# Performance work log

Hardware: AMD Instinct MI355X
Metric: run time of the kernel (lower is better)

Reference implementation:

```python
import jax, jax.numpy as jnp
import numpy as np

INPUT_DIM = 2048
OUT_DIM = 4096
DEGREE = 3          # repo's 'degree' arg; acts as spline ORDER (recursion depth degree-1)
N_KNOTS = 64
N_COEF = N_KNOTS - DEGREE  # 61, matches c.shape[-1]


def bspline_basis(x, t, order):
    """Vectorized Cox-de Boor. x: (I,), t: (K,) -> basis (I, K - order).

    Degree-0 indicators then `order-1` recursion steps, matching the
    original per-scalar recursive cox_deboor(c, t, order, x) whose output
    length is n_knots - order (== c.shape[-1]).
    """
    xk = x[:, None]  # (I, 1)
    # B_{k,0}(x) = 1 if t[k] <= x < t[k+1]   -> (I, K-1)
    B = ((t[None, :-1] <= xk) & (xk < t[None, 1:])).astype(x.dtype)
    for p in range(1, order):
        # left:  (x - t[k]) / (t[k+p] - t[k])
        left = (xk - t[None, : -(p + 1)]) / (t[p:-1] - t[: -(p + 1)])[None, :]
        # right: (t[k+p+1] - x) / (t[k+p+1] - t[k+1])
        right = (t[None, p + 1 :] - xk) / (t[p + 1 :] - t[1 : t.shape[0] - p])[None, :]
        B = left * B[:, :-1] + right * B[:, 1:]
    return B  # (I, K - order)


def setup_inputs() -> dict:
    key = jax.random.key(0)
    kx, kc = jax.random.split(key)
    x = jax.random.uniform(kx, (INPUT_DIM,), dtype=jnp.float32)  # in [0,1) c [-1,1]
    c = jax.random.normal(kc, (INPUT_DIM, OUT_DIM, N_COEF), dtype=jnp.float32)
    return {"x": x, "c": c}


def reference(x, c):
    t = jnp.linspace(-1.0, 1.0, N_KNOTS, dtype=x.dtype)
    B = bspline_basis(x, t, DEGREE)           # (I, N_COEF)
    # out[j] = sum_i sum_k c[i,j,k] * B[i,k]
    return jnp.einsum("iok,ik->o", c, B)       # (OUT_DIM,)
```

## Files before the change

### kernel.cpp

```cpp
#include <hip/hip_runtime.h>
#include <math.h>


#define INPUT_DIM 2048
#define OUT_DIM   4096
#define N_COEF    61
#define IC        16
#define OB        256

__device__ __forceinline__ float Tk(int k) {
    return -1.0f + (float)k * (2.0f / 63.0f);
}

__global__ void kan_zero_kernel(float* __restrict__ out) {
    out[blockIdx.x * blockDim.x + threadIdx.x] = 0.0f;
}

__global__ __launch_bounds__(OB) void kan_kernel(const float* __restrict__ x,
                                                 const float* __restrict__ c,
                                                 float* __restrict__ out) {
    __shared__ int    sk0[IC];
    __shared__ float4 sw[IC];

    const int tid    = threadIdx.x;
    const int i_base = blockIdx.y * IC;

    if (tid < IC) {
        const float xv = x[i_base + tid];
        int j = (int)floorf((xv + 1.0f) * 31.5f);
        j = max(0, min(62, j));
        while (j > 0  && xv <  Tk(j))     --j;
        while (j < 62 && xv >= Tk(j + 1)) ++j;

        const float tjm1 = Tk(j - 1), tj = Tk(j), tj1 = Tk(j + 1), tj2 = Tk(j + 2);
        const float b1l = (tj1 - xv) / (tj1 - tj);
        const float b1r = (xv - tj)  / (tj1 - tj);
        const float w0 = (tj1 - xv) / (tj1 - tjm1) * b1l;
        const float w1 = (xv - tjm1) / (tj1 - tjm1) * b1l
                       + (tj2 - xv) / (tj2 - tj)    * b1r;
        const float w2 = (xv - tj)  / (tj2 - tj)    * b1r;

        int s = j - 59; if (s < 0) s = 0;
        int k0 = j - 2 - s; if (k0 < 0) k0 = 0;
        const float wsrc[3] = {w0, w1, w2};
        float ww[4] = {0.0f, 0.0f, 0.0f, 0.0f};
        #pragma unroll
        for (int m = 0; m < 3; ++m) {
            const int l = (j - 2 + m) - k0;
            if (0 <= l && l < 4) ww[l] = wsrc[m];
        }
        sk0[tid] = k0;
        sw[tid]  = make_float4(ww[0], ww[1], ww[2], ww[3]);
    }
    __syncthreads();

    const int o = blockIdx.x * OB + tid;
    const long long stride_i = (long long)OUT_DIM * N_COEF;
    const float* pbase = c + (long long)i_base * stride_i + (long long)o * N_COEF;

    float4 d[IC];
    #pragma unroll
    for (int ii = 0; ii < IC; ++ii) {
        const float* p = pbase + (long long)ii * stride_i + sk0[ii];
        d[ii] = *reinterpret_cast<const float4*>(p);
    }

    float acc = 0.0f;
    #pragma unroll
    for (int ii = 0; ii < IC; ++ii) {
        const float4 w = sw[ii];
        acc = fmaf(d[ii].x, w.x, acc);
        acc = fmaf(d[ii].y, w.y, acc);
        acc = fmaf(d[ii].z, w.z, acc);
        acc = fmaf(d[ii].w, w.w, acc);
    }
    atomicAdd(&out[o], acc);
}

extern "C" void kernel_launch(void* const* d_in, const int* in_sizes, int n_in,
                              void* d_out, int out_size, void* d_ws, size_t ws_size,
                              hipStream_t stream) {
    const float* x   = (const float*)d_in[0];
    const float* c   = (const float*)d_in[1];
    float*       out = (float*)d_out;

    hipLaunchKernelGGL(kan_zero_kernel, dim3(OUT_DIM / 256), dim3(256), 0, stream, out);

    dim3 grid(OUT_DIM / OB, INPUT_DIM / IC);
    hipLaunchKernelGGL(kan_kernel, grid, dim3(OB), 0, stream, x, c, out);
}
```

Baseline: 2.356 ms.

## Stream full coefficient chunks through LDS with coalesced loads instead of sparse gathers

Replaces the per-thread sparse float4 gather of 4 coefficients (strided by 61 floats) with a fully coalesced copy of each 256x61 coefficient chunk into shared memory, then reads the 4 needed values from LDS. It also doubles the input rows per block from 16 to 32, which halves the number of atomics. The gather wasted sector bandwidth and coalescing, but the new version reads all 61 coefficients per output instead of about 4, roughly 15x more DRAM traffic. It also adds two barriers per row with no overlap between loading and compute.

New measurement: 2.668 ms. 1.13x slower.

```diff
diff --git a/kernel.cpp b/kernel.cpp
--- a/kernel.cpp
+++ b/kernel.cpp
@@ -5,8 +5,10 @@
 #define INPUT_DIM 2048
 #define OUT_DIM   4096
 #define N_COEF    61
-#define IC        16
 #define OB        256
+#define IG        32
+#define CHUNK_F   (OB * N_COEF)
+#define CHUNK_V4  (CHUNK_F / 4)
 
 __device__ __forceinline__ float Tk(int k) {
     return -1.0f + (float)k * (2.0f / 63.0f);
@@ -19,13 +21,15 @@
 __global__ __launch_bounds__(OB) void kan_kernel(const float* __restrict__ x,
                                                  const float* __restrict__ c,
                                                  float* __restrict__ out) {
-    __shared__ int    sk0[IC];
-    __shared__ float4 sw[IC];
+    __shared__ float4 ldsv[CHUNK_V4];
+    __shared__ int    sk0[IG];
+    __shared__ float4 sw[IG];
 
     const int tid    = threadIdx.x;
-    const int i_base = blockIdx.y * IC;
+    const int o0     = blockIdx.x * OB;
+    const int i_base = blockIdx.y * IG;
 
-    if (tid < IC) {
+    if (tid < IG) {
         const float xv = x[i_base + tid];
         int j = (int)floorf((xv + 1.0f) * 31.5f);
         j = max(0, min(62, j));
@@ -54,27 +58,28 @@
     }
     __syncthreads();
 
-    const int o = blockIdx.x * OB + tid;
-    const long long stride_i = (long long)OUT_DIM * N_COEF;
-    const float* pbase = c + (long long)i_base * stride_i + (long long)o * N_COEF;
+    const float* ldsf = (const float*)ldsv;
+    float acc = 0.0f;
 
-    float4 d[IC];
-    #pragma unroll
-    for (int ii = 0; ii < IC; ++ii) {
-        const float* p = pbase + (long long)ii * stride_i + sk0[ii];
-        d[ii] = *reinterpret_cast<const float4*>(p);
+    for (int ii = 0; ii < IG; ++ii) {
+        const float4* src = (const float4*)(c + ((long long)(i_base + ii) * OUT_DIM + o0)
+                                                  * (long long)N_COEF);
+        for (int idx = tid; idx < CHUNK_V4; idx += OB) {
+            ldsv[idx] = src[idx];
+        }
+        __syncthreads();
+
+        const int    k0 = sk0[ii];
+        const float4 w  = sw[ii];
+        const float* row = ldsf + tid * N_COEF + k0;
+        acc = fmaf(row[0], w.x, acc);
+        acc = fmaf(row[1], w.y, acc);
+        acc = fmaf(row[2], w.z, acc);
+        acc = fmaf(row[3], w.w, acc);
+        __syncthreads();
     }
 
-    float acc = 0.0f;
-    #pragma unroll
-    for (int ii = 0; ii < IC; ++ii) {
-        const float4 w = sw[ii];
-        acc = fmaf(d[ii].x, w.x, acc);
-        acc = fmaf(d[ii].y, w.y, acc);
-        acc = fmaf(d[ii].z, w.z, acc);
-        acc = fmaf(d[ii].w, w.w, acc);
-    }
-    atomicAdd(&out[o], acc);
+    atomicAdd(&out[o0 + tid], acc);
 }
 
 extern "C" void kernel_launch(void* const* d_in, const int* in_sizes, int n_in,
@@ -86,6 +91,6 @@
 
     hipLaunchKernelGGL(kan_zero_kernel, dim3(OUT_DIM / 256), dim3(256), 0, stream, out);
 
-    dim3 grid(OUT_DIM / OB, INPUT_DIM / IC);
+    dim3 grid(OUT_DIM / OB, INPUT_DIM / IG);
     hipLaunchKernelGGL(kan_kernel, grid, dim3(OB), 0, stream, x, c, out);
 }
```
